# Performance work log

Measured on AMD Instinct MI355X. Metric: run time of the kernel, lower is better.

## Reference

```python
import jax, jax.numpy as jnp
import numpy as np

N = 50000   # nodes
E = 800000  # edges (avg degree 16)
G = 256     # graphs in batch
IN = 64; H = 128; K = 8; C = 10; L = 3
TAU = 1.0


def _bn(x, g, b, eps=1e-5):
    # BatchNorm1d training-mode forward: batch stats over the row dim.
    m = x.mean(0)
    v = x.var(0)
    return (x - m) * jax.lax.rsqrt(v + eps) * g + b


def _ln(x, g, b, eps=1e-5):
    m = x.mean(-1, keepdims=True)
    v = x.var(-1, keepdims=True)
    return (x - m) * jax.lax.rsqrt(v + eps) * g + b


def setup_inputs() -> dict:
    key = jax.random.key(0)
    ks = jax.random.split(key, 16)
    p = lambda k, shape: jax.random.normal(k, shape, jnp.float32) * 0.05
    u = jax.random.uniform(ks[2], (N, K), minval=1e-10, maxval=1.0)
    return {
        "x": jax.random.normal(ks[0], (N, IN), jnp.float32),
        "edge_index": jax.random.randint(ks[1], (2, E), 0, N, dtype=jnp.int32),
        "batch": (jnp.arange(N, dtype=jnp.int32) * G) // N,  # sorted, all graphs present
        "gumbel": -jnp.log(-jnp.log(u)),  # fixed Gumbel(0,1) noise
        "inp_w": p(ks[3], (IN, H)), "inp_b": jnp.zeros(H),
        "elin_w": p(ks[4], (L, 1, H)), "elin_b": jnp.zeros((L, H)),
        "mlp1_w": p(ks[5], (L, H, H)), "mlp1_b": jnp.zeros((L, H)),
        "mlpbn_g": jnp.ones((L, H)), "mlpbn_b": jnp.zeros((L, H)),
        "mlp2_w": p(ks[6], (L, H, H)), "mlp2_b": jnp.zeros((L, H)),
        "bn_g": jnp.ones((L, H)), "bn_b": jnp.zeros((L, H)),
        "bh1_w": p(ks[7], (H, H // 2)), "bh1_b": jnp.zeros(H // 2),
        "bh2_w": p(ks[8], (H // 2, K)), "bh2_b": jnp.zeros(K),
        "bm_w": p(ks[9], (H, H)), "bm_b": jnp.zeros(H),
        "ln_g": jnp.ones(H), "ln_b": jnp.zeros(H),
        "clf1_w": p(ks[10], (2 * H, H)), "clf1_b": jnp.zeros(H),
        "clfbn_g": jnp.ones(H), "clfbn_b": jnp.zeros(H),
        "clf2_w": p(ks[11], (H, C)), "clf2_b": jnp.zeros(C),
    }


def reference(x, edge_index, batch, gumbel, inp_w, inp_b, elin_w, elin_b,
              mlp1_w, mlp1_b, mlpbn_g, mlpbn_b, mlp2_w, mlp2_b, bn_g, bn_b,
              bh1_w, bh1_b, bh2_w, bh2_b, bm_w, bm_b, ln_g, ln_b,
              clf1_w, clf1_b, clfbn_g, clfbn_b, clf2_w, clf2_b):
    src, dst = edge_index[0], edge_index[1]
    h = x @ inp_w + inp_b  # [N,H]
    for l in range(L):  # GINEConv stack (eps=0, dummy edge attr = ones[E,1])
        e_emb = elin_w[l][0] + elin_b[l]          # ones @ W + b -> single [H] vector
        msg = jax.nn.relu(h[src] + e_emb)          # gather + add, [E,H]
        aggr = jax.ops.segment_sum(msg, dst, num_segments=N)  # scatter-add
        z = h + aggr                               # (1+eps)*x + aggr, eps=0
        z = jax.nn.relu(_bn(z @ mlp1_w[l] + mlp1_b[l], mlpbn_g[l], mlpbn_b[l]))
        z = z @ mlp2_w[l] + mlp2_b[l]
        h = jax.nn.relu(_bn(z, bn_g[l], bn_b[l]))
    # blob assignment via gumbel-softmax (soft)
    logits = jax.nn.relu(h @ bh1_w + bh1_b) @ bh2_w + bh2_b  # [N,K]
    assign = jax.nn.softmax((logits + gumbel) / TAU, axis=-1)
    counts = jax.ops.segment_sum(jnp.ones((N,), h.dtype), batch, num_segments=G)
    gmean = jax.ops.segment_sum(h, batch, num_segments=G) / counts[:, None]  # [G,H]
    # per-graph weighted blob pooling, vectorized over graphs via segment_sum
    num = jax.ops.segment_sum(assign[:, :, None] * h[:, None, :], batch, num_segments=G)  # [G,K,H]
    den = jax.ops.segment_sum(assign, batch, num_segments=G)  # [G,K]
    blobs = num / (den[:, :, None] + 1e-8)
    blobs = _ln(jax.nn.relu(blobs @ bm_w + bm_b), ln_g, ln_b)
    blob_emb = blobs.max(axis=1)  # [G,H]
    z = jnp.concatenate([gmean, blob_emb], axis=-1)  # [G,2H]
    z = jax.nn.relu(_bn(z @ clf1_w + clf1_b, clfbn_g, clfbn_b))
    return z @ clf2_w + clf2_b  # [G,C]
```

## Files before the change

### kernel.cpp

```cpp
#include <hip/hip_runtime.h>
#include <hip/hip_bf16.h>


#define HH 128
typedef unsigned short u16;
typedef unsigned int u32;
typedef __attribute__((ext_vector_type(8))) short bf16x8;
typedef __attribute__((ext_vector_type(4))) float f32x4;

__device__ __forceinline__ void atomAddF(float* p, float v) { unsafeAtomicAdd(p, v); }

__device__ __forceinline__ u16 f2bf(float f) {
    u32 u = __float_as_uint(f);
    u += 0x7fffu + ((u >> 16) & 1u);
    return (u16)(u >> 16);
}
__device__ __forceinline__ float bf2f_lo(u32 u) { return __uint_as_float(u << 16); }
__device__ __forceinline__ float bf2f_hi(u32 u) { return __uint_as_float(u & 0xffff0000u); }
__device__ __forceinline__ void split2(float v, u16& hi, u16& lo) {
    u16 h_ = f2bf(v);
    float hf = __uint_as_float(((u32)h_) << 16);
    hi = h_;
    lo = f2bf(v - hf);
}
__device__ __forceinline__ u32 swz(u32 row, u32 kByte, u32 strideB) {
    return (row * strideB + kByte) ^ ((row & 7u) << 4);
}

#define WTOT (8192 + 6 * 16384)

__global__ void k_prep(const float* __restrict__ inp_w, const float* __restrict__ m1,
                       const float* __restrict__ m2, u16* __restrict__ Whi,
                       u16* __restrict__ Wlo) {
    int b = blockIdx.x;
    int t = threadIdx.x;
    if (b == 0) {
        for (int idx = t; idx < 128 * 64; idx += 256) {
            int c = idx >> 6, k = idx & 63;
            u16 hi, lo;
            split2(inp_w[k * 128 + c], hi, lo);
            Whi[idx] = hi; Wlo[idx] = lo;
        }
    } else {
        const float* W = (b <= 3) ? m1 + (size_t)(b - 1) * 16384
                                  : m2 + (size_t)(b - 4) * 16384;
        u16* dh = Whi + 8192 + (size_t)(b - 1) * 16384;
        u16* dl = Wlo + 8192 + (size_t)(b - 1) * 16384;
        for (int idx = t; idx < 16384; idx += 256) {
            int c = idx >> 7, k = idx & 127;
            u16 hi, lo;
            split2(W[k * 128 + c], hi, lo);
            dh[idx] = hi; dl[idx] = lo;
        }
    }
}

__global__ void k_hist(const int* __restrict__ ei, int* __restrict__ deg, int E) {
    int i4 = blockIdx.x * 256 + threadIdx.x;
    int e0 = i4 * 4;
    if (e0 + 3 < E) {
        int4 d = *(const int4*)(ei + E + e0);
        atomicAdd(&deg[d.x], 1);
        atomicAdd(&deg[d.y], 1);
        atomicAdd(&deg[d.z], 1);
        atomicAdd(&deg[d.w], 1);
    } else {
        for (int e = e0; e < E; e++) atomicAdd(&deg[ei[E + e]], 1);
    }
}

__global__ void k_bsum(const int* __restrict__ deg, int* __restrict__ bsum, int N) {
    int t = threadIdx.x;
    int i = blockIdx.x * 256 + t;
    int v = (i < N) ? deg[i] : 0;
    for (int o = 32; o; o >>= 1) v += __shfl_down(v, o);
    __shared__ int ws_[4];
    if ((t & 63) == 0) ws_[t >> 6] = v;
    __syncthreads();
    if (t == 0) bsum[blockIdx.x] = ws_[0] + ws_[1] + ws_[2] + ws_[3];
}

__global__ void k_scan1(const int* __restrict__ bsum, int* __restrict__ boff,
                        int* __restrict__ rowptrN, int nch) {
    int t = threadIdx.x;
    int v = (t < nch) ? bsum[t] : 0;
    int l = t & 63, w = t >> 6;
    int sv = v;
    for (int o = 1; o < 64; o <<= 1) { int u = __shfl_up(sv, o); if (l >= o) sv += u; }
    __shared__ int wsum[4];
    if (l == 63) wsum[w] = sv;
    __syncthreads();
    int add = 0;
    for (int j = 0; j < w; j++) add += wsum[j];
    if (t < nch) boff[t] = sv - v + add;
    if (t == nch - 1) *rowptrN = sv + add;
}

__global__ void k_scan2(const int* __restrict__ deg, const int* __restrict__ boff,
                        int* __restrict__ rowptr, int* __restrict__ cursor, int N) {
    int b = blockIdx.x, t = threadIdx.x, i = b * 256 + t;
    int v = (i < N) ? deg[i] : 0;
    int l = t & 63, w = t >> 6;
    int sv = v;
    for (int o = 1; o < 64; o <<= 1) { int u = __shfl_up(sv, o); if (l >= o) sv += u; }
    __shared__ int wsum[4];
    if (l == 63) wsum[w] = sv;
    __syncthreads();
    int add = boff[b];
    for (int j = 0; j < w; j++) add += wsum[j];
    if (i < N) { int e = sv - v + add; rowptr[i] = e; cursor[i] = e; }
}

__global__ void k_fill(const int* __restrict__ ei, int* __restrict__ cursor,
                       int* __restrict__ col, int E) {
    int i4 = blockIdx.x * 256 + threadIdx.x;
    int e0 = i4 * 4;
    if (e0 + 3 < E) {
        int4 s = *(const int4*)(ei + e0);
        int4 d = *(const int4*)(ei + E + e0);
        int p0 = atomicAdd(&cursor[d.x], 1);
        int p1 = atomicAdd(&cursor[d.y], 1);
        int p2 = atomicAdd(&cursor[d.z], 1);
        int p3 = atomicAdd(&cursor[d.w], 1);
        col[p0] = s.x;
        col[p1] = s.y;
        col[p2] = s.z;
        col[p3] = s.w;
    } else {
        for (int e = e0; e < E; e++) {
            int pos = atomicAdd(&cursor[ei[E + e]], 1);
            col[pos] = ei[e];
        }
    }
}

template <int KD, int MODE, bool STATS, bool FOUT, bool BOUT>
__global__ __launch_bounds__(512) void k_mgemm(
    const float* __restrict__ inf, const u16* __restrict__ inhi,
    const u16* __restrict__ inlo, const u16* __restrict__ Whi,
    const u16* __restrict__ Wlo, const float* __restrict__ bias,
    const float* __restrict__ statsIn, const float* __restrict__ gamma,
    const float* __restrict__ beta, float invN,
    float* __restrict__ out, u16* __restrict__ outb,
    float* __restrict__ statsOut, int Nrows, int ntiles) {
    __shared__ u16 s_Bhi[128 * KD];
    __shared__ u16 s_Blo[128 * KD];
    __shared__ float s_red[2][8][128];
    __shared__ float s_sc[128], s_sh[128];
    const int t = threadIdx.x;
    constexpr u32 STR = KD * 2;
    constexpr int KCB = KD / 8;
    constexpr int NB = (128 * KCB) / 512;
    constexpr int NF = KD / 32;

#pragma unroll
    for (int i = 0; i < NB; i++) {
        int idx = i * 512 + t;
        int c = idx / KCB, kc = idx % KCB;
        u32 off = swz(c, kc * 16, STR);
        *(uint4*)((char*)s_Bhi + off) = *(const uint4*)(Whi + (size_t)c * KD + kc * 8);
        *(uint4*)((char*)s_Blo + off) = *(const uint4*)(Wlo + (size_t)c * KD + kc * 8);
    }
    if (MODE == 1 && t < 128) {
        float m = statsIn[t] * invN;
        float var = statsIn[128 + t] * invN - m * m;
        float s = gamma[t] * rsqrtf(var + 1e-5f);
        s_sc[t] = s;
        s_sh[t] = beta[t] - m * s;
    }
    __syncthreads();

    const int l = t & 63, w = t >> 6;
    const int c0 = l & 15;
    const int ksub = (l >> 4) * 8;
    const u32 kOffB = (u32)(l >> 4) * 16u;

    for (int tile = blockIdx.x; tile < ntiles; tile += gridDim.x) {
        const int row = tile * 128 + w * 16 + c0;
        const bool rv = row < Nrows;

        bf16x8 ah[NF], al[NF];
        if (MODE == 2) {
#pragma unroll
            for (int kk = 0; kk < NF; kk++) {
                int k0 = kk * 32 + ksub;
                if (rv) {
                    ah[kk] = *(const bf16x8*)(inhi + (size_t)row * KD + k0);
                    al[kk] = *(const bf16x8*)(inlo + (size_t)row * KD + k0);
                } else {
                    uint4 z = {0, 0, 0, 0};
                    ah[kk] = *(bf16x8*)&z;
                    al[kk] = *(bf16x8*)&z;
                }
            }
        } else {
#pragma unroll
            for (int kk = 0; kk < NF; kk++) {
                int k0 = kk * 32 + ksub;
                float4 v0 = {0.f, 0.f, 0.f, 0.f}, v1 = {0.f, 0.f, 0.f, 0.f};
                if (rv) {
                    v0 = *(const float4*)(inf + (size_t)row * KD + k0);
                    v1 = *(const float4*)(inf + (size_t)row * KD + k0 + 4);
                }
                float vv[8] = {v0.x, v0.y, v0.z, v0.w, v1.x, v1.y, v1.z, v1.w};
                uint4 uh, ul;
                u32* ph = (u32*)&uh;
                u32* pl = (u32*)&ul;
#pragma unroll
                for (int p = 0; p < 4; p++) {
                    float a0 = vv[2 * p], a1 = vv[2 * p + 1];
                    if (MODE == 1) {
                        a0 = fmaxf(a0 * s_sc[k0 + 2 * p] + s_sh[k0 + 2 * p], 0.f);
                        a1 = fmaxf(a1 * s_sc[k0 + 2 * p + 1] + s_sh[k0 + 2 * p + 1], 0.f);
                    }
                    u16 h0, l0, h1, l1;
                    split2(a0, h0, l0);
                    split2(a1, h1, l1);
                    ph[p] = (u32)h0 | ((u32)h1 << 16);
                    pl[p] = (u32)l0 | ((u32)l1 << 16);
                }
                ah[kk] = *(bf16x8*)&uh;
                al[kk] = *(bf16x8*)&ul;
            }
        }

        f32x4 acc[8];
#pragma unroll
        for (int n = 0; n < 8; n++) acc[n] = (f32x4){0.f, 0.f, 0.f, 0.f};
#pragma unroll
        for (int kk = 0; kk < NF; kk++) {
            u32 kb = kk * 64 + kOffB;
#pragma unroll
            for (int n = 0; n < 8; n++) {
                u32 ob = swz(n * 16 + c0, kb, STR);
                bf16x8 bh = *(const bf16x8*)((char*)s_Bhi + ob);
                bf16x8 bl = *(const bf16x8*)((char*)s_Blo + ob);
                acc[n] = __builtin_amdgcn_mfma_f32_16x16x32_bf16(ah[kk], bh, acc[n], 0, 0, 0);
                acc[n] = __builtin_amdgcn_mfma_f32_16x16x32_bf16(al[kk], bh, acc[n], 0, 0, 0);
                acc[n] = __builtin_amdgcn_mfma_f32_16x16x32_bf16(ah[kk], bl, acc[n], 0, 0, 0);
            }
        }

        const int rbase = tile * 128 + w * 16 + ((l >> 4) << 2);
#pragma unroll
        for (int n = 0; n < 8; n++) {
            const int colc = n * 16 + c0;
            const float bv = bias[colc];
            float s = 0.f, q = 0.f;
#pragma unroll
            for (int j = 0; j < 4; j++) {
                int gr = rbase + j;
                if (gr < Nrows) {
                    float v = acc[n][j] + bv;
                    if (FOUT) out[(size_t)gr * HH + colc] = v;
                    if (BOUT) outb[(size_t)gr * HH + colc] = f2bf(v);
                    s += v;
                    q += v * v;
                }
            }
            if (STATS) {
                s += __shfl_xor(s, 16); s += __shfl_xor(s, 32);
                q += __shfl_xor(q, 16); q += __shfl_xor(q, 32);
                if (l < 16) {
                    s_red[0][w][n * 16 + l] = s;
                    s_red[1][w][n * 16 + l] = q;
                }
            }
        }
        if (STATS) {
            __syncthreads();
            if (t < 128) {
                float S = 0.f, Q = 0.f;
#pragma unroll
                for (int ww = 0; ww < 8; ww++) { S += s_red[0][ww][t]; Q += s_red[1][ww][t]; }
                atomAddF(&statsOut[t], S);
                atomAddF(&statsOut[HH + t], Q);
            }
            __syncthreads();
        }
    }
}

template <int BN>
__global__ __launch_bounds__(256) void k_gather(
    const u16* __restrict__ act,
    const int* __restrict__ rowptr, const int* __restrict__ col,
    const float* __restrict__ ew, const float* __restrict__ eb,
    const float* __restrict__ stats, const float* __restrict__ gamma,
    const float* __restrict__ beta, float invN,
    u16* __restrict__ zhi, u16* __restrict__ zlo, int N) {
    __shared__ float2 s_part[2][64];
    const int wv = threadIdx.x >> 6;
    const int lane = threadIdx.x & 63;
    const int node = blockIdx.x * 2 + (wv >> 1);
    const int hf = wv & 1;
    const int c2 = lane * 2;
    float2 acc = {0.f, 0.f};
    const bool valid = node < N;
    float2 ee = {0.f, 0.f};
    float sc0 = 1.f, sh0 = 0.f, sc1 = 1.f, sh1 = 0.f;
    if (BN) {
        float m0 = stats[c2] * invN;
        float v0 = stats[128 + c2] * invN - m0 * m0;
        sc0 = gamma[c2] * rsqrtf(v0 + 1e-5f);
        sh0 = beta[c2] - m0 * sc0;
        float m1 = stats[c2 + 1] * invN;
        float v1 = stats[128 + c2 + 1] * invN - m1 * m1;
        sc1 = gamma[c2 + 1] * rsqrtf(v1 + 1e-5f);
        sh1 = beta[c2 + 1] - m1 * sc1;
    }
    auto proc = [&](u32 u) {
        float v0 = bf2f_lo(u), v1 = bf2f_hi(u);
        if (BN) {
            v0 = fmaxf(fmaf(v0, sc0, sh0), 0.f);
            v1 = fmaxf(fmaf(v1, sc1, sh1), 0.f);
        }
        acc.x += fmaxf(v0 + ee.x, 0.f);
        acc.y += fmaxf(v1 + ee.y, 0.f);
    };
    if (valid) {
        ee.x = ew[c2] + eb[c2];
        ee.y = ew[c2 + 1] + eb[c2 + 1];
        const int s = rowptr[node], eend = rowptr[node + 1];
        int e = s + hf;
        for (; e + 14 < eend; e += 16) {
            int s0 = col[e], s1 = col[e + 2], s2 = col[e + 4], s3 = col[e + 6];
            int s4 = col[e + 8], s5 = col[e + 10], s6 = col[e + 12], s7 = col[e + 14];
            u32 u0 = *(const u32*)(act + (size_t)s0 * HH + c2);
            u32 u1 = *(const u32*)(act + (size_t)s1 * HH + c2);
            u32 u2 = *(const u32*)(act + (size_t)s2 * HH + c2);
            u32 u3 = *(const u32*)(act + (size_t)s3 * HH + c2);
            u32 u4 = *(const u32*)(act + (size_t)s4 * HH + c2);
            u32 u5 = *(const u32*)(act + (size_t)s5 * HH + c2);
            u32 u6 = *(const u32*)(act + (size_t)s6 * HH + c2);
            u32 u7 = *(const u32*)(act + (size_t)s7 * HH + c2);
            proc(u0); proc(u1); proc(u2); proc(u3);
            proc(u4); proc(u5); proc(u6); proc(u7);
        }
        for (; e + 6 < eend; e += 8) {
            int s0 = col[e], s1 = col[e + 2], s2 = col[e + 4], s3 = col[e + 6];
            u32 u0 = *(const u32*)(act + (size_t)s0 * HH + c2);
            u32 u1 = *(const u32*)(act + (size_t)s1 * HH + c2);
            u32 u2 = *(const u32*)(act + (size_t)s2 * HH + c2);
            u32 u3 = *(const u32*)(act + (size_t)s3 * HH + c2);
            proc(u0); proc(u1); proc(u2); proc(u3);
        }
        for (; e < eend; e += 2) {
            u32 u0 = *(const u32*)(act + (size_t)col[e] * HH + c2);
            proc(u0);
        }
    }
    if (hf) s_part[wv >> 1][lane] = acc;
    __syncthreads();
    if (!hf && valid) {
        float2 p = s_part[wv >> 1][lane];
        u32 un = *(const u32*)(act + (size_t)node * HH + c2);
        float s0 = bf2f_lo(un), s1 = bf2f_hi(un);
        if (BN) {
            s0 = fmaxf(fmaf(s0, sc0, sh0), 0.f);
            s1 = fmaxf(fmaf(s1, sc1, sh1), 0.f);
        }
        float zx = s0 + acc.x + p.x;
        float zy = s1 + acc.y + p.y;
        u16 h0, h1, l0, l1;
        split2(zx, h0, l0);
        split2(zy, h1, l1);
        *(u32*)(zhi + (size_t)node * HH + c2) = (u32)h0 | ((u32)h1 << 16);
        *(u32*)(zlo + (size_t)node * HH + c2) = (u32)l0 | ((u32)l1 << 16);
    }
}

__global__ void k_bnrelu(const float* __restrict__ t, const float* __restrict__ stats,
                         const float* __restrict__ g, const float* __restrict__ b,
                         float invN, float* __restrict__ h, int total4) {
    int i = blockIdx.x * 256 + threadIdx.x;
    if (i >= total4) return;
    int c4 = (i & 31) << 2;
    float sc[4], sh[4];
#pragma unroll
    for (int j = 0; j < 4; j++) {
        float m = stats[c4 + j] * invN;
        float var = stats[128 + c4 + j] * invN - m * m;
        float s = g[c4 + j] * rsqrtf(var + 1e-5f);
        sc[j] = s;
        sh[j] = b[c4 + j] - m * s;
    }
    float4 v = *(const float4*)(t + (size_t)i * 4);
    float4 o;
    o.x = fmaxf(v.x * sc[0] + sh[0], 0.f);
    o.y = fmaxf(v.y * sc[1] + sh[1], 0.f);
    o.z = fmaxf(v.z * sc[2] + sh[2], 0.f);
    o.w = fmaxf(v.w * sc[3] + sh[3], 0.f);
    *(float4*)(h + (size_t)i * 4) = o;
}

__global__ __launch_bounds__(256) void k_assign(
    const float* __restrict__ h, const float* __restrict__ gum,
    const float* __restrict__ w1, const float* __restrict__ b1,
    const float* __restrict__ w2, const float* __restrict__ b2,
    float* __restrict__ assign, int N) {
    __shared__ float s_w1[128 * 64];
    __shared__ float s_w2[64 * 8];
    __shared__ float s_h[32][128];
    __shared__ float s_hid[32][64];
    const int t = threadIdx.x;
    const int n0 = blockIdx.x * 32;
    for (int i = t; i < 128 * 64; i += 256) s_w1[i] = w1[i];
    for (int i = t; i < 512; i += 256) s_w2[i] = w2[i];
    for (int i = t; i < 32 * 32; i += 256) {
        int r = i >> 5, c4 = (i & 31) << 2;
        int gn = n0 + r;
        float4 v = {0.f, 0.f, 0.f, 0.f};
        if (gn < N) v = *(const float4*)(h + (size_t)gn * HH + c4);
        *(float4*)(&s_h[r][c4]) = v;
    }
    __syncthreads();
    for (int o = t; o < 32 * 64; o += 256) {
        int nn = o >> 6, j = o & 63;
        float acc = b1[j];
        for (int k = 0; k < 128; k++) acc = fmaf(s_h[nn][k], s_w1[k * 64 + j], acc);
        s_hid[nn][j] = fmaxf(acc, 0.f);
    }
    __syncthreads();
    int nn = t >> 3, kk = t & 7;
    int gn = n0 + nn;
    float a = b2[kk];
    for (int j = 0; j < 64; j++) a = fmaf(s_hid[nn][j], s_w2[j * 8 + kk], a);
    if (gn < N) a += gum[(size_t)gn * 8 + kk];
    float m = a;
    m = fmaxf(m, __shfl_xor(m, 1));
    m = fmaxf(m, __shfl_xor(m, 2));
    m = fmaxf(m, __shfl_xor(m, 4));
    float e = expf(a - m);
    float s = e;
    s += __shfl_xor(s, 1); s += __shfl_xor(s, 2); s += __shfl_xor(s, 4);
    if (gn < N) assign[(size_t)gn * 8 + kk] = e / s;
}

__device__ __forceinline__ int lowerb(const int* __restrict__ arr, int n, int val) {
    int lo = 0, hi = n;
    while (lo < hi) {
        int mid = (lo + hi) >> 1;
        if (arr[mid] < val) lo = mid + 1;
        else hi = mid;
    }
    return lo;
}

__global__ __launch_bounds__(1024) void k_tail(
    const float* __restrict__ h, const float* __restrict__ assign,
    const int* __restrict__ batch, const float* __restrict__ bm_w,
    const float* __restrict__ bm_b, const float* __restrict__ ln_g,
    const float* __restrict__ ln_b, const float* __restrict__ clf1_w,
    const float* __restrict__ clf1_b, float* __restrict__ t4,
    float* __restrict__ stats, int N) {
    __shared__ float4 s_num[4][8][32];
    __shared__ float4 s_gm[4][32];
    __shared__ float s_den[4][8];
    __shared__ float s_numf[8][128];
    __shared__ float s_denf[8];
    __shared__ float s_blob[8][128];
    __shared__ float s_cat[256];
    __shared__ float s_r[16][2];
    const int g = blockIdx.x;
    const int t = threadIdx.x;
    const int ns = t >> 8;
    const int k = (t >> 5) & 7;
    const int lane = t & 31;
    const int c4 = lane << 2;
    const int start = lowerb(batch, N, g);
    const int end = lowerb(batch, N, g + 1);

    float4 an = {0.f, 0.f, 0.f, 0.f};
    float4 gm = {0.f, 0.f, 0.f, 0.f};
    float ad = 0.f;
    for (int n = start + ns; n < end; n += 4) {
        float a = assign[(size_t)n * 8 + k];
        const float4 hv = *(const float4*)(h + (size_t)n * HH + c4);
        an.x = fmaf(a, hv.x, an.x);
        an.y = fmaf(a, hv.y, an.y);
        an.z = fmaf(a, hv.z, an.z);
        an.w = fmaf(a, hv.w, an.w);
        if (k == 0) { gm.x += hv.x; gm.y += hv.y; gm.z += hv.z; gm.w += hv.w; }
        ad += a;
    }
    s_num[ns][k][lane] = an;
    if (k == 0) s_gm[ns][lane] = gm;
    if (lane == 0) s_den[ns][k] = ad;
    __syncthreads();
    if (t < 256) {
        float4 a0 = s_num[0][k][lane], a1 = s_num[1][k][lane];
        float4 a2 = s_num[2][k][lane], a3 = s_num[3][k][lane];
        s_numf[k][c4 + 0] = a0.x + a1.x + a2.x + a3.x;
        s_numf[k][c4 + 1] = a0.y + a1.y + a2.y + a3.y;
        s_numf[k][c4 + 2] = a0.z + a1.z + a2.z + a3.z;
        s_numf[k][c4 + 3] = a0.w + a1.w + a2.w + a3.w;
        if (t < 32) {
            float4 g0 = s_gm[0][lane], g1 = s_gm[1][lane];
            float4 g2 = s_gm[2][lane], g3 = s_gm[3][lane];
            int cnt = end - start;
            float inv = 1.f / (float)(cnt > 0 ? cnt : 1);
            s_cat[c4 + 0] = (g0.x + g1.x + g2.x + g3.x) * inv;
            s_cat[c4 + 1] = (g0.y + g1.y + g2.y + g3.y) * inv;
            s_cat[c4 + 2] = (g0.z + g1.z + g2.z + g3.z) * inv;
            s_cat[c4 + 3] = (g0.w + g1.w + g2.w + g3.w) * inv;
        }
        if (t < 8) s_denf[t] = s_den[0][t] + s_den[1][t] + s_den[2][t] + s_den[3][t];
    }
    __syncthreads();

    {
        const int kk = t >> 7;
        const int c = t & 127;
        const float d = 1.f / (s_denf[kk] + 1e-8f);
        float acc = bm_b[c];
        for (int j = 0; j < 128; j++)
            acc = fmaf(s_numf[kk][j] * d, bm_w[j * HH + c], acc);
        float y = fmaxf(acc, 0.f);
        float s = y, q = y * y;
        for (int off = 32; off > 0; off >>= 1) {
            s += __shfl_down(s, off);
            q += __shfl_down(q, off);
        }
        const int wv = t >> 6;
        if ((t & 63) == 0) { s_r[wv][0] = s; s_r[wv][1] = q; }
        __syncthreads();
        float S = s_r[kk * 2][0] + s_r[kk * 2 + 1][0];
        float Q = s_r[kk * 2][1] + s_r[kk * 2 + 1][1];
        float m = S * (1.f / 128.f);
        float var = Q * (1.f / 128.f) - m * m;
        s_blob[kk][c] = (y - m) * rsqrtf(var + 1e-5f) * ln_g[c] + ln_b[c];
    }
    __syncthreads();

    if (t < 128) {
        float m = s_blob[0][t];
#pragma unroll
        for (int kk = 1; kk < 8; kk++) m = fmaxf(m, s_blob[kk][t]);
        s_cat[128 + t] = m;
    }
    __syncthreads();

    if (t < 128) {
        float acc = clf1_b[t];
        for (int j = 0; j < 256; j++) acc = fmaf(s_cat[j], clf1_w[j * HH + t], acc);
        t4[(size_t)g * HH + t] = acc;
        atomAddF(&stats[t], acc);
        atomAddF(&stats[HH + t], acc * acc);
    }
}

__global__ void k_clf2(const float* __restrict__ t4, const float* __restrict__ stats,
                       const float* __restrict__ g_, const float* __restrict__ b_,
                       float invG, const float* __restrict__ w,
                       const float* __restrict__ bias, float* __restrict__ out) {
    int g = blockIdx.x;
    int t = threadIdx.x;
    __shared__ float s[128];
    float m = stats[t] * invG;
    float var = stats[128 + t] * invG - m * m;
    float sc = g_[t] * rsqrtf(var + 1e-5f);
    float sh = b_[t] - m * sc;
    s[t] = fmaxf(t4[(size_t)g * HH + t] * sc + sh, 0.f);
    __syncthreads();
    if (t < 10) {
        float acc = bias[t];
        for (int j = 0; j < 128; j++) acc = fmaf(s[j], w[j * 10 + t], acc);
        out[(size_t)g * 10 + t] = acc;
    }
}

extern "C" void kernel_launch(void* const* d_in, const int* in_sizes, int n_in,
                              void* d_out, int out_size, void* d_ws, size_t ws_size,
                              hipStream_t stream) {
    const float* x      = (const float*)d_in[0];
    const int*   ei     = (const int*)d_in[1];
    const int*   batch  = (const int*)d_in[2];
    const float* gumbel = (const float*)d_in[3];
    const float* inp_w  = (const float*)d_in[4];
    const float* inp_b  = (const float*)d_in[5];
    const float* elin_w = (const float*)d_in[6];
    const float* elin_b = (const float*)d_in[7];
    const float* mlp1_w = (const float*)d_in[8];
    const float* mlp1_b = (const float*)d_in[9];
    const float* mlpbn_g = (const float*)d_in[10];
    const float* mlpbn_b = (const float*)d_in[11];
    const float* mlp2_w = (const float*)d_in[12];
    const float* mlp2_b = (const float*)d_in[13];
    const float* bn_g   = (const float*)d_in[14];
    const float* bn_b   = (const float*)d_in[15];
    const float* bh1_w  = (const float*)d_in[16];
    const float* bh1_b  = (const float*)d_in[17];
    const float* bh2_w  = (const float*)d_in[18];
    const float* bh2_b  = (const float*)d_in[19];
    const float* bm_w   = (const float*)d_in[20];
    const float* bm_b   = (const float*)d_in[21];
    const float* ln_g   = (const float*)d_in[22];
    const float* ln_b   = (const float*)d_in[23];
    const float* clf1_w = (const float*)d_in[24];
    const float* clf1_b = (const float*)d_in[25];
    const float* clfbn_g = (const float*)d_in[26];
    const float* clfbn_b = (const float*)d_in[27];
    const float* clf2_w = (const float*)d_in[28];
    const float* clf2_b = (const float*)d_in[29];
    float* out = (float*)d_out;

    const int N = in_sizes[0] / 64;
    const int E = in_sizes[1] / 2;
    const int G = out_size / 10;

    float* ws = (float*)d_ws;
    float* A      = ws;
    float* B      = A + (size_t)N * HH;
    float* C      = B + (size_t)N * HH;
    float* assign = C + (size_t)N * HH;
    float* t4     = assign + (size_t)N * 8;
    float* statsA = t4 + (size_t)G * HH;
    u16* Whi = (u16*)(statsA + 7 * 256);
    u16* Wlo = Whi + WTOT;
    int* rowptr = (int*)(Wlo + WTOT);
    int* cursor = rowptr + (N + 1);
    int* colidx = cursor + N;
    int* bsum   = colidx + E;
    int* boff   = bsum + 256;
    u16* zhi  = (u16*)A;
    u16* zlo  = zhi + (size_t)N * HH;
    float* h  = A;
    u16* t2b  = (u16*)B;
    float* t2f = B;
    u16* act0 = (u16*)C;
    float* t1 = C;

    const dim3 B256(256), B128(128), B512(512), B1024(1024);
    const int ntiles = (N + 127) / 128;
    const int gg = ntiles < 512 ? ntiles : 512;
    const int nch = (N + 255) / 256;
    const int e4 = (E + 4 * 256 - 1) / (4 * 256);
    const float invN = 1.f / (float)N;
    const float invG = 1.f / (float)G;

    k_prep<<<7, B256, 0, stream>>>(inp_w, mlp1_w, mlp2_w, Whi, Wlo);
    hipMemsetAsync(cursor, 0, (size_t)N * sizeof(int), stream);
    hipMemsetAsync(statsA, 0, 7 * 256 * sizeof(float), stream);
    k_hist<<<e4, B256, 0, stream>>>(ei, cursor, E);
    k_bsum<<<nch, B256, 0, stream>>>(cursor, bsum, N);
    k_scan1<<<1, B256, 0, stream>>>(bsum, boff, rowptr + N, nch);
    k_scan2<<<nch, B256, 0, stream>>>(cursor, boff, rowptr, cursor, N);
    k_fill<<<e4, B256, 0, stream>>>(ei, cursor, colidx, E);

    k_mgemm<64, 0, false, false, true><<<gg, B512, 0, stream>>>(
        x, nullptr, nullptr, Whi, Wlo, inp_b, nullptr, nullptr, nullptr, 0.f,
        nullptr, act0, nullptr, N, ntiles);

    for (int l = 0; l < 3; l++) {
        float* sa = statsA + (size_t)(2 * l) * 256;
        float* sb = sa + 256;
        if (l == 0)
            k_gather<0><<<(N + 1) / 2, B256, 0, stream>>>(
                act0, rowptr, colidx, elin_w, elin_b,
                nullptr, nullptr, nullptr, 0.f, zhi, zlo, N);
        else
            k_gather<1><<<(N + 1) / 2, B256, 0, stream>>>(
                t2b, rowptr, colidx, elin_w + l * HH, elin_b + l * HH,
                statsA + (size_t)(2 * (l - 1) + 1) * 256,
                bn_g + (l - 1) * HH, bn_b + (l - 1) * HH, invN, zhi, zlo, N);
        k_mgemm<128, 2, true, true, false><<<gg, B512, 0, stream>>>(
            nullptr, zhi, zlo, Whi + 8192 + (size_t)l * 16384,
            Wlo + 8192 + (size_t)l * 16384, mlp1_b + l * HH,
            nullptr, nullptr, nullptr, 0.f, t1, nullptr, sa, N, ntiles);
        if (l < 2)
            k_mgemm<128, 1, true, false, true><<<gg, B512, 0, stream>>>(
                t1, nullptr, nullptr, Whi + 8192 + (size_t)(3 + l) * 16384,
                Wlo + 8192 + (size_t)(3 + l) * 16384, mlp2_b + l * HH,
                sa, mlpbn_g + l * HH, mlpbn_b + l * HH, invN,
                nullptr, t2b, sb, N, ntiles);
        else
            k_mgemm<128, 1, true, true, false><<<gg, B512, 0, stream>>>(
                t1, nullptr, nullptr, Whi + 8192 + (size_t)(3 + l) * 16384,
                Wlo + 8192 + (size_t)(3 + l) * 16384, mlp2_b + l * HH,
                sa, mlpbn_g + l * HH, mlpbn_b + l * HH, invN,
                t2f, nullptr, sb, N, ntiles);
    }
    k_bnrelu<<<(N * 32 + 255) / 256, B256, 0, stream>>>(
        t2f, statsA + 5 * 256, bn_g + 2 * HH, bn_b + 2 * HH, invN, h, N * 32);

    k_assign<<<(N + 31) / 32, B256, 0, stream>>>(h, gumbel, bh1_w, bh1_b, bh2_w, bh2_b, assign, N);
    float* sc_ = statsA + 6 * 256;
    k_tail<<<G, B1024, 0, stream>>>(h, assign, batch, bm_w, bm_b, ln_g, ln_b,
                                    clf1_w, clf1_b, t4, sc_, N);
    k_clf2<<<G, B128, 0, stream>>>(t4, sc_, clfbn_g, clfbn_b, invG, clf2_w, clf2_b, out);
}
```

Before: 501.4 us.

## Read GEMM weights from global memory and split BN-ReLU out of gather

The GEMM kernel no longer stages the hi/lo bf16 weight tiles in swizzled shared memory. Each MFMA operand is now read straight from global memory through the cache. Separately, the previous layer's BatchNorm+ReLU is taken out of the gather kernel and run as a standalone bf16 elementwise kernel that writes normalized activations, so gather just sums neighbours. This removes LDS staging, one barrier and per-edge normalization math, but adds repeated global weight loads inside the MFMA loop and an extra pass over activations per layer.

Result: slower. 768.9 us (+53.4%).

```diff
diff --git a/kernel.cpp b/kernel.cpp
--- a/kernel.cpp
+++ b/kernel.cpp
@@ -22,9 +22,6 @@
     float hf = __uint_as_float(((u32)h_) << 16);
     hi = h_;
     lo = f2bf(v - hf);
-}
-__device__ __forceinline__ u32 swz(u32 row, u32 kByte, u32 strideB) {
-    return (row * strideB + kByte) ^ ((row & 7u) << 4);
 }
 
 #define WTOT (8192 + 6 * 16384)
@@ -143,24 +140,11 @@
     const float* __restrict__ beta, float invN,
     float* __restrict__ out, u16* __restrict__ outb,
     float* __restrict__ statsOut, int Nrows, int ntiles) {
-    __shared__ u16 s_Bhi[128 * KD];
-    __shared__ u16 s_Blo[128 * KD];
     __shared__ float s_red[2][8][128];
     __shared__ float s_sc[128], s_sh[128];
     const int t = threadIdx.x;
-    constexpr u32 STR = KD * 2;
-    constexpr int KCB = KD / 8;
-    constexpr int NB = (128 * KCB) / 512;
     constexpr int NF = KD / 32;
 
-#pragma unroll
-    for (int i = 0; i < NB; i++) {
-        int idx = i * 512 + t;
-        int c = idx / KCB, kc = idx % KCB;
-        u32 off = swz(c, kc * 16, STR);
-        *(uint4*)((char*)s_Bhi + off) = *(const uint4*)(Whi + (size_t)c * KD + kc * 8);
-        *(uint4*)((char*)s_Blo + off) = *(const uint4*)(Wlo + (size_t)c * KD + kc * 8);
-    }
     if (MODE == 1 && t < 128) {
         float m = statsIn[t] * invN;
         float var = statsIn[128 + t] * invN - m * m;
@@ -168,12 +152,11 @@
         s_sc[t] = s;
         s_sh[t] = beta[t] - m * s;
     }
-    __syncthreads();
+    if (MODE == 1) __syncthreads();
 
     const int l = t & 63, w = t >> 6;
     const int c0 = l & 15;
     const int ksub = (l >> 4) * 8;
-    const u32 kOffB = (u32)(l >> 4) * 16u;
 
     for (int tile = blockIdx.x; tile < ntiles; tile += gridDim.x) {
         const int row = tile * 128 + w * 16 + c0;
@@ -229,12 +212,12 @@
         for (int n = 0; n < 8; n++) acc[n] = (f32x4){0.f, 0.f, 0.f, 0.f};
 #pragma unroll
         for (int kk = 0; kk < NF; kk++) {
-            u32 kb = kk * 64 + kOffB;
+            int k0 = kk * 32 + ksub;
 #pragma unroll
             for (int n = 0; n < 8; n++) {
-                u32 ob = swz(n * 16 + c0, kb, STR);
-                bf16x8 bh = *(const bf16x8*)((char*)s_Bhi + ob);
-                bf16x8 bl = *(const bf16x8*)((char*)s_Blo + ob);
+                const size_t boff = (size_t)(n * 16 + c0) * KD + k0;
+                bf16x8 bh = *(const bf16x8*)(Whi + boff);
+                bf16x8 bl = *(const bf16x8*)(Wlo + boff);
                 acc[n] = __builtin_amdgcn_mfma_f32_16x16x32_bf16(ah[kk], bh, acc[n], 0, 0, 0);
                 acc[n] = __builtin_amdgcn_mfma_f32_16x16x32_bf16(al[kk], bh, acc[n], 0, 0, 0);
                 acc[n] = __builtin_amdgcn_mfma_f32_16x16x32_bf16(ah[kk], bl, acc[n], 0, 0, 0);
@@ -281,13 +264,10 @@
     }
 }
 
-template <int BN>
 __global__ __launch_bounds__(256) void k_gather(
-    const u16* __restrict__ act,
+    const u16* __restrict__ hb,
     const int* __restrict__ rowptr, const int* __restrict__ col,
     const float* __restrict__ ew, const float* __restrict__ eb,
-    const float* __restrict__ stats, const float* __restrict__ gamma,
-    const float* __restrict__ beta, float invN,
     u16* __restrict__ zhi, u16* __restrict__ zlo, int N) {
     __shared__ float2 s_part[2][64];
     const int wv = threadIdx.x >> 6;
@@ -298,26 +278,6 @@
     float2 acc = {0.f, 0.f};
     const bool valid = node < N;
     float2 ee = {0.f, 0.f};
-    float sc0 = 1.f, sh0 = 0.f, sc1 = 1.f, sh1 = 0.f;
-    if (BN) {
-        float m0 = stats[c2] * invN;
-        float v0 = stats[128 + c2] * invN - m0 * m0;
-        sc0 = gamma[c2] * rsqrtf(v0 + 1e-5f);
-        sh0 = beta[c2] - m0 * sc0;
-        float m1 = stats[c2 + 1] * invN;
-        float v1 = stats[128 + c2 + 1] * invN - m1 * m1;
-        sc1 = gamma[c2 + 1] * rsqrtf(v1 + 1e-5f);
-        sh1 = beta[c2 + 1] - m1 * sc1;
-    }
-    auto proc = [&](u32 u) {
-        float v0 = bf2f_lo(u), v1 = bf2f_hi(u);
-        if (BN) {
-            v0 = fmaxf(fmaf(v0, sc0, sh0), 0.f);
-            v1 = fmaxf(fmaf(v1, sc1, sh1), 0.f);
-        }
-        acc.x += fmaxf(v0 + ee.x, 0.f);
-        acc.y += fmaxf(v1 + ee.y, 0.f);
-    };
     if (valid) {
         ee.x = ew[c2] + eb[c2];
         ee.y = ew[c2 + 1] + eb[c2 + 1];
@@ -326,48 +286,78 @@
         for (; e + 14 < eend; e += 16) {
             int s0 = col[e], s1 = col[e + 2], s2 = col[e + 4], s3 = col[e + 6];
             int s4 = col[e + 8], s5 = col[e + 10], s6 = col[e + 12], s7 = col[e + 14];
-            u32 u0 = *(const u32*)(act + (size_t)s0 * HH + c2);
-            u32 u1 = *(const u32*)(act + (size_t)s1 * HH + c2);
-            u32 u2 = *(const u32*)(act + (size_t)s2 * HH + c2);
-            u32 u3 = *(const u32*)(act + (size_t)s3 * HH + c2);
-            u32 u4 = *(const u32*)(act + (size_t)s4 * HH + c2);
-            u32 u5 = *(const u32*)(act + (size_t)s5 * HH + c2);
-            u32 u6 = *(const u32*)(act + (size_t)s6 * HH + c2);
-            u32 u7 = *(const u32*)(act + (size_t)s7 * HH + c2);
-            proc(u0); proc(u1); proc(u2); proc(u3);
-            proc(u4); proc(u5); proc(u6); proc(u7);
+            u32 u0 = *(const u32*)(hb + (size_t)s0 * HH + c2);
+            u32 u1 = *(const u32*)(hb + (size_t)s1 * HH + c2);
+            u32 u2 = *(const u32*)(hb + (size_t)s2 * HH + c2);
+            u32 u3 = *(const u32*)(hb + (size_t)s3 * HH + c2);
+            u32 u4 = *(const u32*)(hb + (size_t)s4 * HH + c2);
+            u32 u5 = *(const u32*)(hb + (size_t)s5 * HH + c2);
+            u32 u6 = *(const u32*)(hb + (size_t)s6 * HH + c2);
+            u32 u7 = *(const u32*)(hb + (size_t)s7 * HH + c2);
+            acc.x += fmaxf(bf2f_lo(u0) + ee.x, 0.f) + fmaxf(bf2f_lo(u1) + ee.x, 0.f) +
+                     fmaxf(bf2f_lo(u2) + ee.x, 0.f) + fmaxf(bf2f_lo(u3) + ee.x, 0.f) +
+                     fmaxf(bf2f_lo(u4) + ee.x, 0.f) + fmaxf(bf2f_lo(u5) + ee.x, 0.f) +
+                     fmaxf(bf2f_lo(u6) + ee.x, 0.f) + fmaxf(bf2f_lo(u7) + ee.x, 0.f);
+            acc.y += fmaxf(bf2f_hi(u0) + ee.y, 0.f) + fmaxf(bf2f_hi(u1) + ee.y, 0.f) +
+                     fmaxf(bf2f_hi(u2) + ee.y, 0.f) + fmaxf(bf2f_hi(u3) + ee.y, 0.f) +
+                     fmaxf(bf2f_hi(u4) + ee.y, 0.f) + fmaxf(bf2f_hi(u5) + ee.y, 0.f) +
+                     fmaxf(bf2f_hi(u6) + ee.y, 0.f) + fmaxf(bf2f_hi(u7) + ee.y, 0.f);
         }
         for (; e + 6 < eend; e += 8) {
             int s0 = col[e], s1 = col[e + 2], s2 = col[e + 4], s3 = col[e + 6];
-            u32 u0 = *(const u32*)(act + (size_t)s0 * HH + c2);
-            u32 u1 = *(const u32*)(act + (size_t)s1 * HH + c2);
-            u32 u2 = *(const u32*)(act + (size_t)s2 * HH + c2);
-            u32 u3 = *(const u32*)(act + (size_t)s3 * HH + c2);
-            proc(u0); proc(u1); proc(u2); proc(u3);
+            u32 u0 = *(const u32*)(hb + (size_t)s0 * HH + c2);
+            u32 u1 = *(const u32*)(hb + (size_t)s1 * HH + c2);
+            u32 u2 = *(const u32*)(hb + (size_t)s2 * HH + c2);
+            u32 u3 = *(const u32*)(hb + (size_t)s3 * HH + c2);
+            acc.x += fmaxf(bf2f_lo(u0) + ee.x, 0.f) + fmaxf(bf2f_lo(u1) + ee.x, 0.f) +
+                     fmaxf(bf2f_lo(u2) + ee.x, 0.f) + fmaxf(bf2f_lo(u3) + ee.x, 0.f);
+            acc.y += fmaxf(bf2f_hi(u0) + ee.y, 0.f) + fmaxf(bf2f_hi(u1) + ee.y, 0.f) +
+                     fmaxf(bf2f_hi(u2) + ee.y, 0.f) + fmaxf(bf2f_hi(u3) + ee.y, 0.f);
         }
         for (; e < eend; e += 2) {
-            u32 u0 = *(const u32*)(act + (size_t)col[e] * HH + c2);
-            proc(u0);
+            u32 u0 = *(const u32*)(hb + (size_t)col[e] * HH + c2);
+            acc.x += fmaxf(bf2f_lo(u0) + ee.x, 0.f);
+            acc.y += fmaxf(bf2f_hi(u0) + ee.y, 0.f);
         }
     }
     if (hf) s_part[wv >> 1][lane] = acc;
     __syncthreads();
     if (!hf && valid) {
         float2 p = s_part[wv >> 1][lane];
-        u32 un = *(const u32*)(act + (size_t)node * HH + c2);
-        float s0 = bf2f_lo(un), s1 = bf2f_hi(un);
-        if (BN) {
-            s0 = fmaxf(fmaf(s0, sc0, sh0), 0.f);
-            s1 = fmaxf(fmaf(s1, sc1, sh1), 0.f);
-        }
-        float zx = s0 + acc.x + p.x;
-        float zy = s1 + acc.y + p.y;
+        u32 un = *(const u32*)(hb + (size_t)node * HH + c2);
+        float zx = bf2f_lo(un) + acc.x + p.x;
+        float zy = bf2f_hi(un) + acc.y + p.y;
         u16 h0, h1, l0, l1;
         split2(zx, h0, l0);
         split2(zy, h1, l1);
         *(u32*)(zhi + (size_t)node * HH + c2) = (u32)h0 | ((u32)h1 << 16);
         *(u32*)(zlo + (size_t)node * HH + c2) = (u32)l0 | ((u32)l1 << 16);
     }
+}
+
+__global__ void k_bnrelu_bf(const u16* __restrict__ tb, const float* __restrict__ stats,
+                            const float* __restrict__ g, const float* __restrict__ b,
+                            float invN, u16* __restrict__ hb, int total4) {
+    int i = blockIdx.x * 256 + threadIdx.x;
+    if (i >= total4) return;
+    int c4 = (i & 31) << 2;
+    float sc[4], sh[4];
+#pragma unroll
+    for (int j = 0; j < 4; j++) {
+        float m = stats[c4 + j] * invN;
+        float var = stats[128 + c4 + j] * invN - m * m;
+        float s = g[c4 + j] * rsqrtf(var + 1e-5f);
+        sc[j] = s;
+        sh[j] = b[c4 + j] - m * s;
+    }
+    uint2 v = *(const uint2*)(tb + (size_t)i * 4);
+    float o0 = fmaxf(bf2f_lo(v.x) * sc[0] + sh[0], 0.f);
+    float o1 = fmaxf(bf2f_hi(v.x) * sc[1] + sh[1], 0.f);
+    float o2 = fmaxf(bf2f_lo(v.y) * sc[2] + sh[2], 0.f);
+    float o3 = fmaxf(bf2f_hi(v.y) * sc[3] + sh[3], 0.f);
+    uint2 p = {(u32)f2bf(o0) | ((u32)f2bf(o1) << 16),
+               (u32)f2bf(o2) | ((u32)f2bf(o3) << 16)};
+    *(uint2*)(hb + (size_t)i * 4) = p;
 }
 
 __global__ void k_bnrelu(const float* __restrict__ t, const float* __restrict__ stats,
@@ -628,7 +618,7 @@
     float* h  = A;
     u16* t2b  = (u16*)B;
     float* t2f = B;
-    u16* act0 = (u16*)C;
+    u16* hb   = (u16*)C;
     float* t1 = C;
 
     const dim3 B256(256), B128(128), B512(512), B1024(1024);
@@ -650,39 +640,36 @@
 
     k_mgemm<64, 0, false, false, true><<<gg, B512, 0, stream>>>(
         x, nullptr, nullptr, Whi, Wlo, inp_b, nullptr, nullptr, nullptr, 0.f,
-        nullptr, act0, nullptr, N, ntiles);
+        nullptr, hb, nullptr, N, ntiles);
 
     for (int l = 0; l < 3; l++) {
         float* sa = statsA + (size_t)(2 * l) * 256;
         float* sb = sa + 256;
-        if (l == 0)
-            k_gather<0><<<(N + 1) / 2, B256, 0, stream>>>(
-                act0, rowptr, colidx, elin_w, elin_b,
-                nullptr, nullptr, nullptr, 0.f, zhi, zlo, N);
-        else
-            k_gather<1><<<(N + 1) / 2, B256, 0, stream>>>(
-                t2b, rowptr, colidx, elin_w + l * HH, elin_b + l * HH,
-                statsA + (size_t)(2 * (l - 1) + 1) * 256,
-                bn_g + (l - 1) * HH, bn_b + (l - 1) * HH, invN, zhi, zlo, N);
+        k_gather<<<(N + 1) / 2, B256, 0, stream>>>(hb, rowptr, colidx,
+                                                   elin_w + l * HH, elin_b + l * HH,
+                                                   zhi, zlo, N);
         k_mgemm<128, 2, true, true, false><<<gg, B512, 0, stream>>>(
             nullptr, zhi, zlo, Whi + 8192 + (size_t)l * 16384,
             Wlo + 8192 + (size_t)l * 16384, mlp1_b + l * HH,
             nullptr, nullptr, nullptr, 0.f, t1, nullptr, sa, N, ntiles);
-        if (l < 2)
+        if (l < 2) {
             k_mgemm<128, 1, true, false, true><<<gg, B512, 0, stream>>>(
                 t1, nullptr, nullptr, Whi + 8192 + (size_t)(3 + l) * 16384,
                 Wlo + 8192 + (size_t)(3 + l) * 16384, mlp2_b + l * HH,
                 sa, mlpbn_g + l * HH, mlpbn_b + l * HH, invN,
                 nullptr, t2b, sb, N, ntiles);
-        else
+            k_bnrelu_bf<<<(N * 32 + 255) / 256, B256, 0, stream>>>(
+                t2b, sb, bn_g + l * HH, bn_b + l * HH, invN, hb, N * 32);
+        } else {
             k_mgemm<128, 1, true, true, false><<<gg, B512, 0, stream>>>(
                 t1, nullptr, nullptr, Whi + 8192 + (size_t)(3 + l) * 16384,
                 Wlo + 8192 + (size_t)(3 + l) * 16384, mlp2_b + l * HH,
                 sa, mlpbn_g + l * HH, mlpbn_b + l * HH, invN,
                 t2f, nullptr, sb, N, ntiles);
-    }
-    k_bnrelu<<<(N * 32 + 255) / 256, B256, 0, stream>>>(
-        t2f, statsA + 5 * 256, bn_g + 2 * HH, bn_b + 2 * HH, invN, h, N * 32);
+            k_bnrelu<<<(N * 32 + 255) / 256, B256, 0, stream>>>(
+                t2f, sb, bn_g + l * HH, bn_b + l * HH, invN, h, N * 32);
+        }
+    }
 
     k_assign<<<(N + 31) / 32, B256, 0, stream>>>(h, gumbel, bh1_w, bh1_b, bh2_w, bh2_b, assign, N);
     float* sc_ = statsA + 6 * 256;
```
